# Optimization experiments

Measured on AMD Instinct MI355X. Metric: run time of the kernel, lower is better.

Reference implementation:

```python
import jax, jax.numpy as jnp
import numpy as np

KERNEL_SIZE = 5
GROUP_SIZE = 1
SCALE = 2


def setup_inputs() -> dict:
    key = jax.random.key(0)
    k1, k2 = jax.random.split(key)
    N, C, H, W = 2, 256, 128, 128
    features = jax.random.normal(k1, (N, C, H, W), dtype=jnp.float32)
    masks = jax.random.uniform(
        k2, (N, KERNEL_SIZE * KERNEL_SIZE * GROUP_SIZE, H * SCALE, W * SCALE),
        dtype=jnp.float32)
    return {"features": features, "masks": masks}


def reference(features, masks):
    # CARAFE: content-aware reassembly upsampling.
    # out[n,c,i,j] = sum_{dy,dx} feat[n,c, i//s + dy - r, j//s + dx - r]
    #                * masks[n, g*K*K + dy*K + dx, i, j]
    K, G, s = KERNEL_SIZE, GROUP_SIZE, SCALE
    N, C, H, W = features.shape
    Cg = C // G
    K2 = K * K
    r = K // 2
    # zero-pad spatially and gather all K*K shifted views -> (N, C, K2, H, W)
    fp = jnp.pad(features, ((0, 0), (0, 0), (r, r), (r, r)))
    patches = jnp.stack(
        [fp[:, :, dy:dy + H, dx:dx + W] for dy in range(K) for dx in range(K)],
        axis=2)
    patches = patches.reshape(N, G, Cg, K2, H, W)
    # masks at output resolution; split each output pixel into (src_pixel, subpixel)
    m = masks.reshape(N, G, K2, H, s, W, s)
    # weighted reduce over the kernel window, broadcast over channels in group
    out = jnp.einsum('ngckhw,ngkhawb->ngchawb', patches, m)
    return out.reshape(N, C, H * s, W * s)
```

## Files before the change

kernel.cpp:

```cpp
#include <hip/hip_runtime.h>

#define KK 5
#define RR 2
#define SS 2
#define N_ 2
#define C_ 256
#define H_ 128
#define W_ 128
#define H2 (H_*SS)
#define W2 (W_*SS)
#define TH 16
#define TW 16
#define CCHUNK 32
#define PH (TH + 2*RR)
#define PW (TW + 2*RR)

__global__ __launch_bounds__(256) void carafe_kernel(
    const float* __restrict__ feat,
    const float* __restrict__ masks,
    float* __restrict__ out)
{
    __shared__ float patch[PH * PW];

    const int tid = threadIdx.x;
    const int tx = tid & 15;
    const int ty = tid >> 4;
    const int bx = blockIdx.x & 7;
    const int by = blockIdx.x >> 3;
    const int c0 = blockIdx.y * CCHUNK;
    const int n  = blockIdx.z;

    const int i0 = by * TH + ty;
    const int j0 = bx * TW + tx;

    float m[KK * KK][SS][SS];
    const float* mbase = masks + (size_t)n * (KK * KK) * (size_t)(H2 * W2);
    #pragma unroll
    for (int k = 0; k < KK * KK; ++k) {
        #pragma unroll
        for (int a = 0; a < SS; ++a) {
            const float2 mv = *reinterpret_cast<const float2*>(
                mbase + ((size_t)k * H2 + (2 * i0 + a)) * W2 + 2 * j0);
            m[k][a][0] = mv.x;
            m[k][a][1] = mv.y;
        }
    }

    const int gy0 = by * TH - RR;
    const int gx0 = bx * TW - RR;

    for (int cc = 0; cc < CCHUNK; ++cc) {
        const int c = c0 + cc;
        const float* fbase = feat + (size_t)(n * C_ + c) * (H_ * W_);

        __syncthreads();
        for (int idx = tid; idx < PH * PW; idx += 256) {
            const int py = idx / PW;
            const int px = idx - py * PW;
            const int gy = gy0 + py;
            const int gx = gx0 + px;
            float v = 0.f;
            if ((unsigned)gy < (unsigned)H_ && (unsigned)gx < (unsigned)W_)
                v = fbase[gy * W_ + gx];
            patch[idx] = v;
        }
        __syncthreads();

        float acc00 = 0.f, acc01 = 0.f, acc10 = 0.f, acc11 = 0.f;
        #pragma unroll
        for (int dy = 0; dy < KK; ++dy) {
            #pragma unroll
            for (int dx = 0; dx < KK; ++dx) {
                const float v = patch[(ty + dy) * PW + (tx + dx)];
                const int k = dy * KK + dx;
                acc00 += v * m[k][0][0];
                acc01 += v * m[k][0][1];
                acc10 += v * m[k][1][0];
                acc11 += v * m[k][1][1];
            }
        }

        float* obase = out + ((size_t)(n * C_ + c) * H2 + (size_t)(2 * i0)) * W2 + 2 * j0;
        *reinterpret_cast<float2*>(obase)      = make_float2(acc00, acc01);
        *reinterpret_cast<float2*>(obase + W2) = make_float2(acc10, acc11);
    }
}

extern "C" void kernel_launch(void* const* d_in, const int* in_sizes, int n_in,
                              void* d_out, int out_size, void* d_ws, size_t ws_size,
                              hipStream_t stream) {
    const float* feat  = (const float*)d_in[0];
    const float* masks = (const float*)d_in[1];
    float* out = (float*)d_out;

    dim3 grid(( W_ / TW) * (H_ / TH),
              C_ / CCHUNK,
              N_);
    dim3 block(256);
    carafe_kernel<<<grid, block, 0, stream>>>(feat, masks, out);
}
```

Baseline: 57.53 us.

## Load all channel patches into shared memory once and stream masks per tap

```diff
diff --git a/kernel.cpp b/kernel.cpp
--- a/kernel.cpp
+++ b/kernel.cpp
@@ -2,25 +2,27 @@
 
 #define KK 5
 #define RR 2
-#define SS 2
 #define N_ 2
 #define C_ 256
 #define H_ 128
 #define W_ 128
-#define H2 (H_*SS)
-#define W2 (W_*SS)
+#define H2 256
+#define W2 256
 #define TH 16
 #define TW 16
-#define CCHUNK 32
-#define PH (TH + 2*RR)
-#define PW (TW + 2*RR)
+#define CCHUNK 16
+#define PH 20
+#define PW 20
+#define PHPW (PH*PW)
+#define CSTR 20
+#define HW (H_*W_)
 
-__global__ __launch_bounds__(256) void carafe_kernel(
+__global__ __launch_bounds__(256, 4) void carafe_kernel(
     const float* __restrict__ feat,
     const float* __restrict__ masks,
     float* __restrict__ out)
 {
-    __shared__ float patch[PH * PW];
+    __shared__ float patch[PHPW * CSTR];
 
     const int tid = threadIdx.x;
     const int tx = tid & 15;
@@ -32,57 +34,59 @@
 
     const int i0 = by * TH + ty;
     const int j0 = bx * TW + tx;
+    const int gy0 = by * TH - RR;
+    const int gx0 = bx * TW - RR;
 
-    float m[KK * KK][SS][SS];
-    const float* mbase = masks + (size_t)n * (KK * KK) * (size_t)(H2 * W2);
+    const float* fbase = feat + (size_t)(n * C_ + c0) * HW;
     #pragma unroll
-    for (int k = 0; k < KK * KK; ++k) {
+    for (int r = 0; r < (CCHUNK * PHPW) / 256; ++r) {
+        const int idx = tid + r * 256;
+        const int c   = idx / PHPW;
+        const int p   = idx - c * PHPW;
+        const int py  = p / PW;
+        const int px  = p - py * PW;
+        const int gy  = gy0 + py;
+        const int gx  = gx0 + px;
+        float v = 0.f;
+        if ((unsigned)gy < (unsigned)H_ && (unsigned)gx < (unsigned)W_)
+            v = fbase[c * HW + gy * W_ + gx];
+        patch[p * CSTR + c] = v;
+    }
+    __syncthreads();
+
+    float acc[CCHUNK][2][2] = {};
+    const float* mb = masks + ((size_t)n * (KK * KK) * H2 + (size_t)(2 * i0)) * W2 + 2 * j0;
+    const int pbase = (ty * PW + tx) * CSTR;
+
+    #pragma unroll
+    for (int dy = 0; dy < KK; ++dy) {
         #pragma unroll
-        for (int a = 0; a < SS; ++a) {
-            const float2 mv = *reinterpret_cast<const float2*>(
-                mbase + ((size_t)k * H2 + (2 * i0 + a)) * W2 + 2 * j0);
-            m[k][a][0] = mv.x;
-            m[k][a][1] = mv.y;
+        for (int dx = 0; dx < KK; ++dx) {
+            const int k = dy * KK + dx;
+            const float* mk = mb + (size_t)k * (H2 * W2);
+            const float2 m0 = *reinterpret_cast<const float2*>(mk);
+            const float2 m1 = *reinterpret_cast<const float2*>(mk + W2);
+            const int off = pbase + (dy * PW + dx) * CSTR;
+            #pragma unroll
+            for (int cg = 0; cg < CCHUNK / 4; ++cg) {
+                const float4 v = *reinterpret_cast<const float4*>(&patch[off + 4 * cg]);
+                acc[4*cg+0][0][0] += v.x * m0.x;  acc[4*cg+0][0][1] += v.x * m0.y;
+                acc[4*cg+0][1][0] += v.x * m1.x;  acc[4*cg+0][1][1] += v.x * m1.y;
+                acc[4*cg+1][0][0] += v.y * m0.x;  acc[4*cg+1][0][1] += v.y * m0.y;
+                acc[4*cg+1][1][0] += v.y * m1.x;  acc[4*cg+1][1][1] += v.y * m1.y;
+                acc[4*cg+2][0][0] += v.z * m0.x;  acc[4*cg+2][0][1] += v.z * m0.y;
+                acc[4*cg+2][1][0] += v.z * m1.x;  acc[4*cg+2][1][1] += v.z * m1.y;
+                acc[4*cg+3][0][0] += v.w * m0.x;  acc[4*cg+3][0][1] += v.w * m0.y;
+                acc[4*cg+3][1][0] += v.w * m1.x;  acc[4*cg+3][1][1] += v.w * m1.y;
+            }
         }
     }
 
-    const int gy0 = by * TH - RR;
-    const int gx0 = bx * TW - RR;
-
-    for (int cc = 0; cc < CCHUNK; ++cc) {
-        const int c = c0 + cc;
-        const float* fbase = feat + (size_t)(n * C_ + c) * (H_ * W_);
-
-        __syncthreads();
-        for (int idx = tid; idx < PH * PW; idx += 256) {
-            const int py = idx / PW;
-            const int px = idx - py * PW;
-            const int gy = gy0 + py;
-            const int gx = gx0 + px;
-            float v = 0.f;
-            if ((unsigned)gy < (unsigned)H_ && (unsigned)gx < (unsigned)W_)
-                v = fbase[gy * W_ + gx];
-            patch[idx] = v;
-        }
-        __syncthreads();
-
-        float acc00 = 0.f, acc01 = 0.f, acc10 = 0.f, acc11 = 0.f;
-        #pragma unroll
-        for (int dy = 0; dy < KK; ++dy) {
-            #pragma unroll
-            for (int dx = 0; dx < KK; ++dx) {
-                const float v = patch[(ty + dy) * PW + (tx + dx)];
-                const int k = dy * KK + dx;
-                acc00 += v * m[k][0][0];
-                acc01 += v * m[k][0][1];
-                acc10 += v * m[k][1][0];
-                acc11 += v * m[k][1][1];
-            }
-        }
-
-        float* obase = out + ((size_t)(n * C_ + c) * H2 + (size_t)(2 * i0)) * W2 + 2 * j0;
-        *reinterpret_cast<float2*>(obase)      = make_float2(acc00, acc01);
-        *reinterpret_cast<float2*>(obase + W2) = make_float2(acc10, acc11);
+    #pragma unroll
+    for (int c = 0; c < CCHUNK; ++c) {
+        float* ob = out + ((size_t)(n * C_ + c0 + c) * H2 + (size_t)(2 * i0)) * W2 + 2 * j0;
+        *reinterpret_cast<float2*>(ob)      = make_float2(acc[c][0][0], acc[c][0][1]);
+        *reinterpret_cast<float2*>(ob + W2) = make_float2(acc[c][1][0], acc[c][1][1]);
     }
 }
 
@@ -93,9 +97,8 @@
     const float* masks = (const float*)d_in[1];
     float* out = (float*)d_out;
 
-    dim3 grid(( W_ / TW) * (H_ / TH),
+    dim3 grid((W_ / TW) * (H_ / TH),
               C_ / CCHUNK,
               N_);
-    dim3 block(256);
-    carafe_kernel<<<grid, block, 0, stream>>>(feat, masks, out);
+    carafe_kernel<<<grid, dim3(256), 0, stream>>>(feat, masks, out);
 }
```

After: 73.41 us. 1.28x slower.
